# Performance work log

Measured on AMD Instinct MI355X. Metric: run time of the kernel, lower is better.

## Reference

```python
import jax, jax.numpy as jnp
import numpy as np

EPS = 1e-3  # freq_scaling_eps default

def _mean_transf(mu, sigma, w, p):
    return jnp.exp(-0.5 * (sigma * w) ** 2) * jnp.sin(p + mu * w)

def _var_transf(mu, sigma, w, p):
    return 0.5 - 0.5 * jnp.exp(-2 * (sigma * w) ** 2) * jnp.cos(2 * (p + mu * w)) - _mean_transf(mu, sigma, w, p) ** 2

def setup_inputs() -> dict:
    key = jax.random.key(0)
    k1, k2, k3, k4 = jax.random.split(key, 4)
    B, IN, F, OUT = 8192, 512, 64, 512
    x = jax.random.normal(k1, (B, IN), dtype=jnp.float32)
    freqs = jax.random.normal(k2, (1, 1, F), dtype=jnp.float32)  # normal(stddev=1.0) init
    phases = jnp.zeros((1, 1, F), dtype=jnp.float32)             # zeros init
    # variance_scaling(1.0,'fan_in',uniform): limit = sqrt(3/fan_in)
    lim_b = np.sqrt(3.0 / F)
    beta = jax.random.uniform(k3, (F, OUT), dtype=jnp.float32, minval=-lim_b, maxval=lim_b)
    lim_l = np.sqrt(3.0 / IN)
    lamb = jax.random.uniform(k4, (IN, OUT), dtype=jnp.float32, minval=-lim_l, maxval=lim_l)
    bias = jnp.zeros((OUT,), dtype=jnp.float32)
    return {"x": x, "freqs": freqs, "phases": phases, "beta": beta, "lamb": lamb, "bias": bias}

def reference(x, freqs, phases, beta, lamb, bias):
    # x: [B, I]; freqs/phases: [1, 1, F]; beta: [F, O]; lamb: [I, O]; bias: [O]
    xb = jnp.sin(freqs * x[:, :, None] + phases)  # [B, I, F]
    mean = _mean_transf(0.0, 1.0, freqs, phases)  # [1, 1, F]
    var = _var_transf(0.0, 1.0, freqs, phases)    # [1, 1, F]
    xb = (xb - mean) / jnp.sqrt(EPS + var)
    out = jnp.einsum('bif,fo,io->bo', xb, beta, lamb)  # bilinear contraction
    return out + bias
```

## Files before the change

### kernel.cpp

```cpp
#include <hip/hip_runtime.h>
#include <hip/hip_bf16.h>


#define TB 256

typedef __attribute__((ext_vector_type(8))) short short8;
typedef __attribute__((ext_vector_type(4))) float floatx4;
typedef __attribute__((ext_vector_type(2))) unsigned int uintx2;
typedef __attribute__((ext_vector_type(4))) unsigned int uintx4;

__device__ __forceinline__ unsigned pk_bf16(float a, float b) {
    union { float f; unsigned u; } ca, cb;
    ca.f = a; cb.f = b;
    unsigned ua = ca.u + 0x8000u;
    unsigned ub = cb.u + 0x8000u;
    return __builtin_amdgcn_perm(ub, ua, 0x07060302u);
}

__device__ __forceinline__ uintx2 sin_pack4(const float xv[4], float wfr, float pfr) {
    float s[4];
    #pragma unroll
    for (int j = 0; j < 4; ++j) {
        float tt = fmaf(xv[j], wfr, pfr);
        float u = tt - __builtin_rintf(tt);
        s[j] = __builtin_amdgcn_sinf(u);
    }
    uintx2 r;
    r.x = pk_bf16(s[0], s[1]);
    r.y = pk_bf16(s[2], s[3]);
    return r;
}

__global__ __launch_bounds__(TB, 2)
void actlayer_kernel(const float* __restrict__ x,
                     const float* __restrict__ freqs,
                     const float* __restrict__ phases,
                     const float* __restrict__ beta,
                     const float* __restrict__ lamb,
                     const float* __restrict__ bias,
                     float* __restrict__ out)
{
    constexpr int I = 512, F = 64, O = 512;
    const int t  = threadIdx.x;
    const int m0 = blockIdx.x * 16;

    __shared__ __align__(16) unsigned short A_sh[2][2][16][72];
    __shared__ __align__(16) unsigned short L_sh[256][72];
    __shared__ float wrev_sh[F], prev_sh[F], r_sh[F], m_sh[F];
    __shared__ float c_sh[512];

    if (t < F) {
        float wq = freqs[t];
        float ph = phases[t];
        float e1 = expf(-0.5f * wq * wq);
        float mean = e1 * sinf(ph);
        float e2 = expf(-2.0f * wq * wq);
        float var = 0.5f - 0.5f * e2 * cosf(2.0f * ph) - mean * mean;
        float r = 1.0f / sqrtf(1e-3f + var);
        wrev_sh[t] = wq * 0.15915494309189535f;
        prev_sh[t] = ph * 0.15915494309189535f;
        r_sh[t] = r;
        m_sh[t] = mean;
    }
    __syncthreads();
    #pragma unroll
    for (int j = 0; j < 2; ++j) {
        int col = t + 256 * j;
        float sb = 0.f;
        #pragma unroll 8
        for (int f = 0; f < F; ++f) sb += beta[f * O + col] * (r_sh[f] * m_sh[f]);
        float sl = 0.f;
        #pragma unroll 8
        for (int i = 0; i < I; ++i) sl += lamb[(size_t)i * O + col];
        c_sh[col] = bias[col] - sb * sl;
    }

    const int lane = t & 63;
    const int ng   = t >> 6;
    const int l15  = lane & 15;
    const int quad = lane >> 4;
    const int r0s  = t >> 4;
    const int kqs  = t & 15;

    floatx4 oacc[8];
    #pragma unroll
    for (int nt = 0; nt < 8; ++nt) oacc[nt] = (floatx4){0.f, 0.f, 0.f, 0.f};
    const floatx4 zero4 = (floatx4){0.f, 0.f, 0.f, 0.f};

    const float* bp = beta + ng * 128 + l15;

    #pragma unroll 1
    for (int it = 0; it < 8; ++it) {
        const int i0 = it * 64;
        float xs[4];
        {
            float4 xv = *(const float4*)(x + (size_t)(m0 + r0s) * I + i0 + kqs * 4);
            xs[0] = xv.x; xs[1] = xv.y; xs[2] = xv.z; xs[3] = xv.w;
        }
        {
            const float* lp = lamb + (size_t)i0 * O + t;
            #pragma unroll
            for (int h = 0; h < 2; ++h) {
                float v[32];
                #pragma unroll
                for (int k = 0; k < 32; ++k) v[k] = lp[(size_t)(h * 32 + k) * O];
                #pragma unroll
                for (int rr = 0; rr < 4; ++rr) {
                    uintx4 w4;
                    w4.x = pk_bf16(v[rr*8+0], v[rr*8+1]);
                    w4.y = pk_bf16(v[rr*8+2], v[rr*8+3]);
                    w4.z = pk_bf16(v[rr*8+4], v[rr*8+5]);
                    w4.w = pk_bf16(v[rr*8+6], v[rr*8+7]);
                    *(uintx4*)&L_sh[t][h * 32 + rr * 8] = w4;
                }
            }
        }
        *(uintx2*)&A_sh[0][0][r0s][kqs * 4] = sin_pack4(xs, wrev_sh[0], prev_sh[0]);
        *(uintx2*)&A_sh[0][1][r0s][kqs * 4] = sin_pack4(xs, wrev_sh[1], prev_sh[1]);
        __syncthreads();
        short8 lf[2][8];
        if (ng < 2) {
            #pragma unroll
            for (int kk = 0; kk < 2; ++kk)
                #pragma unroll
                for (int nt = 0; nt < 8; ++nt)
                    lf[kk][nt] = *(const short8*)&L_sh[ng*128 + nt*16 + l15][kk*32 + quad*8];
        }
        __syncthreads();
        {
            const float* lp = lamb + (size_t)i0 * O + 256 + t;
            #pragma unroll
            for (int h = 0; h < 2; ++h) {
                float v[32];
                #pragma unroll
                for (int k = 0; k < 32; ++k) v[k] = lp[(size_t)(h * 32 + k) * O];
                #pragma unroll
                for (int rr = 0; rr < 4; ++rr) {
                    uintx4 w4;
                    w4.x = pk_bf16(v[rr*8+0], v[rr*8+1]);
                    w4.y = pk_bf16(v[rr*8+2], v[rr*8+3]);
                    w4.z = pk_bf16(v[rr*8+4], v[rr*8+5]);
                    w4.w = pk_bf16(v[rr*8+6], v[rr*8+7]);
                    *(uintx4*)&L_sh[t][h * 32 + rr * 8] = w4;
                }
            }
        }
        __syncthreads();
        if (ng >= 2) {
            #pragma unroll
            for (int kk = 0; kk < 2; ++kk)
                #pragma unroll
                for (int nt = 0; nt < 8; ++nt)
                    lf[kk][nt] = *(const short8*)&L_sh[(ng-2)*128 + nt*16 + l15][kk*32 + quad*8];
        }

        float bA[8], bB[8];
        #pragma unroll
        for (int nt = 0; nt < 8; ++nt) {
            bA[nt] = bp[0 * O + nt * 16];
            bB[nt] = bp[1 * O + nt * 16];
        }
        float rA = r_sh[0], rB = r_sh[1];

        int cur = 0;
        #pragma unroll 1
        for (int f = 0; f < F; f += 2) {
            short8 afA0 = *(const short8*)&A_sh[cur][0][l15][quad * 8];
            short8 afA1 = *(const short8*)&A_sh[cur][0][l15][32 + quad * 8];
            short8 afB0 = *(const short8*)&A_sh[cur][1][l15][quad * 8];
            short8 afB1 = *(const short8*)&A_sh[cur][1][l15][32 + quad * 8];
            float brA[8], brB[8];
            #pragma unroll
            for (int q = 0; q < 8; ++q) { brA[q] = bA[q] * rA; brB[q] = bB[q] * rB; }
            const bool more = (f + 2 < F);
            if (more) {
                #pragma unroll
                for (int nt = 0; nt < 8; ++nt) {
                    bA[nt] = bp[(f + 2) * O + nt * 16];
                    bB[nt] = bp[(f + 3) * O + nt * 16];
                }
                rA = r_sh[f + 2]; rB = r_sh[f + 3];
                *(uintx2*)&A_sh[cur ^ 1][0][r0s][kqs * 4] =
                    sin_pack4(xs, wrev_sh[f + 2], prev_sh[f + 2]);
            }
            #pragma unroll
            for (int nt = 0; nt < 8; ++nt) {
                floatx4 s = __builtin_amdgcn_mfma_f32_16x16x32_bf16(
                    afA0, lf[0][nt], zero4, 0, 0, 0);
                s = __builtin_amdgcn_mfma_f32_16x16x32_bf16(
                    afA1, lf[1][nt], s, 0, 0, 0);
                oacc[nt] += brA[nt] * s;
            }
            if (more) {
                *(uintx2*)&A_sh[cur ^ 1][1][r0s][kqs * 4] =
                    sin_pack4(xs, wrev_sh[f + 3], prev_sh[f + 3]);
            }
            #pragma unroll
            for (int nt = 0; nt < 8; ++nt) {
                floatx4 s = __builtin_amdgcn_mfma_f32_16x16x32_bf16(
                    afB0, lf[0][nt], zero4, 0, 0, 0);
                s = __builtin_amdgcn_mfma_f32_16x16x32_bf16(
                    afB1, lf[1][nt], s, 0, 0, 0);
                oacc[nt] += brB[nt] * s;
            }
            __syncthreads();
            cur ^= 1;
        }
    }

    #pragma unroll
    for (int nt = 0; nt < 8; ++nt) {
        int gn = ng * 128 + nt * 16 + l15;
        float cv = c_sh[gn];
        int gm = m0 + quad * 4;
        #pragma unroll
        for (int rg = 0; rg < 4; ++rg) {
            out[(size_t)(gm + rg) * O + gn] = oacc[nt][rg] + cv;
        }
    }
}

extern "C" void kernel_launch(void* const* d_in, const int* in_sizes, int n_in,
                              void* d_out, int out_size, void* d_ws, size_t ws_size,
                              hipStream_t stream) {
    const float* x      = (const float*)d_in[0];
    const float* freqs  = (const float*)d_in[1];
    const float* phases = (const float*)d_in[2];
    const float* beta   = (const float*)d_in[3];
    const float* lamb   = (const float*)d_in[4];
    const float* bias   = (const float*)d_in[5];
    float* out = (float*)d_out;

    dim3 grid(512);
    dim3 block(TB);
    hipLaunchKernelGGL(actlayer_kernel, grid, block, 0, stream,
                       x, freqs, phases, beta, lamb, bias, out);
}
```

Measured before the change: 419.0 us.

## Retile to 32-row by 256-column blocks with 512 threads

Each block now covers 32 rows and half of the output columns instead of 16 rows and all columns. It uses 8 waves arranged as 2 M-groups by 4 N-groups, and launch bounds target 4 blocks per CU. The lambda tile staged per block is halved and each staged lambda fragment is reused across twice as many rows, with fewer accumulators per wave. In exchange, the sine feature tile is recomputed by both column-half blocks, doubling transcendental work. The tighter register budget also risks spills.

```diff
diff --git a/kernel.cpp b/kernel.cpp
--- a/kernel.cpp
+++ b/kernel.cpp
@@ -2,7 +2,7 @@
 #include <hip/hip_bf16.h>
 
 
-#define TB 256
+#define TB 512
 
 typedef __attribute__((ext_vector_type(8))) short short8;
 typedef __attribute__((ext_vector_type(4))) float floatx4;
@@ -31,7 +31,7 @@
     return r;
 }
 
-__global__ __launch_bounds__(TB, 2)
+__global__ __launch_bounds__(TB, 4)
 void actlayer_kernel(const float* __restrict__ x,
                      const float* __restrict__ freqs,
                      const float* __restrict__ phases,
@@ -42,12 +42,16 @@
 {
     constexpr int I = 512, F = 64, O = 512;
     const int t  = threadIdx.x;
-    const int m0 = blockIdx.x * 16;
-
-    __shared__ __align__(16) unsigned short A_sh[2][2][16][72];
-    __shared__ __align__(16) unsigned short L_sh[256][72];
+    const int bx = blockIdx.x;
+    const int bn = bx & 1;
+    const int bm = bx >> 1;
+    const int n0 = bn * 256;
+    const int m0 = bm * 32;
+
+    __shared__ __align__(16) unsigned short A_sh[2][2][32][72];
+    __shared__ __align__(16) unsigned short L_scr[128][72];
     __shared__ float wrev_sh[F], prev_sh[F], r_sh[F], m_sh[F];
-    __shared__ float c_sh[512];
+    __shared__ float c_sh[256];
 
     if (t < F) {
         float wq = freqs[t];
@@ -63,100 +67,97 @@
         m_sh[t] = mean;
     }
     __syncthreads();
-    #pragma unroll
-    for (int j = 0; j < 2; ++j) {
-        int col = t + 256 * j;
+    if (t < 256) {
+        int col = n0 + t;
         float sb = 0.f;
         #pragma unroll 8
         for (int f = 0; f < F; ++f) sb += beta[f * O + col] * (r_sh[f] * m_sh[f]);
         float sl = 0.f;
         #pragma unroll 8
         for (int i = 0; i < I; ++i) sl += lamb[(size_t)i * O + col];
-        c_sh[col] = bias[col] - sb * sl;
+        c_sh[t] = bias[col] - sb * sl;
     }
 
     const int lane = t & 63;
-    const int ng   = t >> 6;
+    const int wid  = t >> 6;
+    const int mg   = wid >> 2;
+    const int ngw  = wid & 3;
     const int l15  = lane & 15;
     const int quad = lane >> 4;
-    const int r0s  = t >> 4;
-    const int kqs  = t & 15;
-
-    floatx4 oacc[8];
+    const int r0s = t >> 4;
+    const int kqs = t & 15;
+    const int cL  = t & 127;
+    const int khL = t >> 7;
+
+    floatx4 oacc[4];
     #pragma unroll
-    for (int nt = 0; nt < 8; ++nt) oacc[nt] = (floatx4){0.f, 0.f, 0.f, 0.f};
+    for (int nt = 0; nt < 4; ++nt) oacc[nt] = (floatx4){0.f, 0.f, 0.f, 0.f};
     const floatx4 zero4 = (floatx4){0.f, 0.f, 0.f, 0.f};
 
-    const float* bp = beta + ng * 128 + l15;
+    const float* bp = beta + n0 + ngw * 64 + l15;
 
     #pragma unroll 1
     for (int it = 0; it < 8; ++it) {
         const int i0 = it * 64;
+        {
+            const float* lp = lamb + (size_t)(i0 + khL * 16) * O + n0 + cL;
+            float v[16];
+            #pragma unroll
+            for (int k = 0; k < 16; ++k) v[k] = lp[(size_t)k * O];
+            #pragma unroll
+            for (int rr = 0; rr < 2; ++rr) {
+                uintx4 w4;
+                w4.x = pk_bf16(v[rr*8+0], v[rr*8+1]);
+                w4.y = pk_bf16(v[rr*8+2], v[rr*8+3]);
+                w4.z = pk_bf16(v[rr*8+4], v[rr*8+5]);
+                w4.w = pk_bf16(v[rr*8+6], v[rr*8+7]);
+                *(uintx4*)&L_scr[cL][khL * 16 + rr * 8] = w4;
+            }
+        }
         float xs[4];
         {
             float4 xv = *(const float4*)(x + (size_t)(m0 + r0s) * I + i0 + kqs * 4);
             xs[0] = xv.x; xs[1] = xv.y; xs[2] = xv.z; xs[3] = xv.w;
         }
+        __syncthreads();
+        short8 lf[2][4];
+        if (ngw < 2) {
+            #pragma unroll
+            for (int kk = 0; kk < 2; ++kk)
+                #pragma unroll
+                for (int nt = 0; nt < 4; ++nt)
+                    lf[kk][nt] = *(const short8*)&L_scr[ngw*64 + nt*16 + l15][kk*32 + quad*8];
+        }
+        __syncthreads();
         {
-            const float* lp = lamb + (size_t)i0 * O + t;
-            #pragma unroll
-            for (int h = 0; h < 2; ++h) {
-                float v[32];
-                #pragma unroll
-                for (int k = 0; k < 32; ++k) v[k] = lp[(size_t)(h * 32 + k) * O];
-                #pragma unroll
-                for (int rr = 0; rr < 4; ++rr) {
-                    uintx4 w4;
-                    w4.x = pk_bf16(v[rr*8+0], v[rr*8+1]);
-                    w4.y = pk_bf16(v[rr*8+2], v[rr*8+3]);
-                    w4.z = pk_bf16(v[rr*8+4], v[rr*8+5]);
-                    w4.w = pk_bf16(v[rr*8+6], v[rr*8+7]);
-                    *(uintx4*)&L_sh[t][h * 32 + rr * 8] = w4;
-                }
+            const float* lp = lamb + (size_t)(i0 + khL * 16) * O + n0 + 128 + cL;
+            float v[16];
+            #pragma unroll
+            for (int k = 0; k < 16; ++k) v[k] = lp[(size_t)k * O];
+            #pragma unroll
+            for (int rr = 0; rr < 2; ++rr) {
+                uintx4 w4;
+                w4.x = pk_bf16(v[rr*8+0], v[rr*8+1]);
+                w4.y = pk_bf16(v[rr*8+2], v[rr*8+3]);
+                w4.z = pk_bf16(v[rr*8+4], v[rr*8+5]);
+                w4.w = pk_bf16(v[rr*8+6], v[rr*8+7]);
+                *(uintx4*)&L_scr[cL][khL * 16 + rr * 8] = w4;
             }
         }
         *(uintx2*)&A_sh[0][0][r0s][kqs * 4] = sin_pack4(xs, wrev_sh[0], prev_sh[0]);
         *(uintx2*)&A_sh[0][1][r0s][kqs * 4] = sin_pack4(xs, wrev_sh[1], prev_sh[1]);
         __syncthreads();
-        short8 lf[2][8];
-        if (ng < 2) {
+        if (ngw >= 2) {
             #pragma unroll
             for (int kk = 0; kk < 2; ++kk)
                 #pragma unroll
-                for (int nt = 0; nt < 8; ++nt)
-                    lf[kk][nt] = *(const short8*)&L_sh[ng*128 + nt*16 + l15][kk*32 + quad*8];
-        }
-        __syncthreads();
-        {
-            const float* lp = lamb + (size_t)i0 * O + 256 + t;
-            #pragma unroll
-            for (int h = 0; h < 2; ++h) {
-                float v[32];
-                #pragma unroll
-                for (int k = 0; k < 32; ++k) v[k] = lp[(size_t)(h * 32 + k) * O];
-                #pragma unroll
-                for (int rr = 0; rr < 4; ++rr) {
-                    uintx4 w4;
-                    w4.x = pk_bf16(v[rr*8+0], v[rr*8+1]);
-                    w4.y = pk_bf16(v[rr*8+2], v[rr*8+3]);
-                    w4.z = pk_bf16(v[rr*8+4], v[rr*8+5]);
-                    w4.w = pk_bf16(v[rr*8+6], v[rr*8+7]);
-                    *(uintx4*)&L_sh[t][h * 32 + rr * 8] = w4;
-                }
-            }
-        }
-        __syncthreads();
-        if (ng >= 2) {
-            #pragma unroll
-            for (int kk = 0; kk < 2; ++kk)
-                #pragma unroll
-                for (int nt = 0; nt < 8; ++nt)
-                    lf[kk][nt] = *(const short8*)&L_sh[(ng-2)*128 + nt*16 + l15][kk*32 + quad*8];
-        }
-
-        float bA[8], bB[8];
+                for (int nt = 0; nt < 4; ++nt)
+                    lf[kk][nt] = *(const short8*)&L_scr[(ngw-2)*64 + nt*16 + l15][kk*32 + quad*8];
+        }
+
+        float bA[4], bB[4];
         #pragma unroll
-        for (int nt = 0; nt < 8; ++nt) {
+        for (int nt = 0; nt < 4; ++nt) {
             bA[nt] = bp[0 * O + nt * 16];
             bB[nt] = bp[1 * O + nt * 16];
         }
@@ -165,17 +166,18 @@
         int cur = 0;
         #pragma unroll 1
         for (int f = 0; f < F; f += 2) {
-            short8 afA0 = *(const short8*)&A_sh[cur][0][l15][quad * 8];
-            short8 afA1 = *(const short8*)&A_sh[cur][0][l15][32 + quad * 8];
-            short8 afB0 = *(const short8*)&A_sh[cur][1][l15][quad * 8];
-            short8 afB1 = *(const short8*)&A_sh[cur][1][l15][32 + quad * 8];
-            float brA[8], brB[8];
-            #pragma unroll
-            for (int q = 0; q < 8; ++q) { brA[q] = bA[q] * rA; brB[q] = bB[q] * rB; }
+            const int arow = mg * 16 + l15;
+            short8 afA0 = *(const short8*)&A_sh[cur][0][arow][quad * 8];
+            short8 afA1 = *(const short8*)&A_sh[cur][0][arow][32 + quad * 8];
+            short8 afB0 = *(const short8*)&A_sh[cur][1][arow][quad * 8];
+            short8 afB1 = *(const short8*)&A_sh[cur][1][arow][32 + quad * 8];
+            float brA[4], brB[4];
+            #pragma unroll
+            for (int q = 0; q < 4; ++q) { brA[q] = bA[q] * rA; brB[q] = bB[q] * rB; }
             const bool more = (f + 2 < F);
             if (more) {
                 #pragma unroll
-                for (int nt = 0; nt < 8; ++nt) {
+                for (int nt = 0; nt < 4; ++nt) {
                     bA[nt] = bp[(f + 2) * O + nt * 16];
                     bB[nt] = bp[(f + 3) * O + nt * 16];
                 }
@@ -184,7 +186,7 @@
                     sin_pack4(xs, wrev_sh[f + 2], prev_sh[f + 2]);
             }
             #pragma unroll
-            for (int nt = 0; nt < 8; ++nt) {
+            for (int nt = 0; nt < 4; ++nt) {
                 floatx4 s = __builtin_amdgcn_mfma_f32_16x16x32_bf16(
                     afA0, lf[0][nt], zero4, 0, 0, 0);
                 s = __builtin_amdgcn_mfma_f32_16x16x32_bf16(
@@ -196,7 +198,7 @@
                     sin_pack4(xs, wrev_sh[f + 3], prev_sh[f + 3]);
             }
             #pragma unroll
-            for (int nt = 0; nt < 8; ++nt) {
+            for (int nt = 0; nt < 4; ++nt) {
                 floatx4 s = __builtin_amdgcn_mfma_f32_16x16x32_bf16(
                     afB0, lf[0][nt], zero4, 0, 0, 0);
                 s = __builtin_amdgcn_mfma_f32_16x16x32_bf16(
@@ -209,10 +211,11 @@
     }
 
     #pragma unroll
-    for (int nt = 0; nt < 8; ++nt) {
-        int gn = ng * 128 + nt * 16 + l15;
-        float cv = c_sh[gn];
-        int gm = m0 + quad * 4;
+    for (int nt = 0; nt < 4; ++nt) {
+        int cn = ngw * 64 + nt * 16 + l15;
+        int gn = n0 + cn;
+        float cv = c_sh[cn];
+        int gm = m0 + mg * 16 + quad * 4;
         #pragma unroll
         for (int rg = 0; rg < 4; ++rg) {
             out[(size_t)(gm + rg) * O + gn] = oacc[nt][rg] + cv;
```

Result: faster. 410.2 us (-2.1%).
